# Performance work log

Hardware: AMD Instinct MI355X
Metric: run time of the kernel (lower is better)

Reference implementation:

```python
import jax, jax.numpy as jnp
import numpy as np

VOXEL_SIZE = np.array([0.2, 0.2, 4.0], dtype=np.float32)
PC_MIN = np.array([0.0, -40.0, -3.0], dtype=np.float32)
BN_EPS = 1e-3
N_POINTS = 1_500_000
N_VOXELS = 200_000
C_IN = 7   # (4 - 3) + 6 stats channels (cluster offset + voxel-center offset)
C_OUT = 64


def setup_inputs() -> dict:
    key = jax.random.key(0)
    ks = jax.random.split(key, 8)
    features = jax.random.normal(ks[0], (N_POINTS, 4), dtype=jnp.float32)
    point2voxel = jax.random.randint(ks[1], (N_POINTS,), 0, N_VOXELS).astype(jnp.int32)
    voxel_coors = jnp.stack([
        jax.random.randint(ks[2], (N_VOXELS,), 0, 2),    # batch idx
        jnp.zeros((N_VOXELS,), jnp.int32),               # z (pillars -> 0)
        jax.random.randint(ks[3], (N_VOXELS,), 0, 400),  # y bin
        jax.random.randint(ks[4], (N_VOXELS,), 0, 352),  # x bin
    ], axis=1).astype(jnp.int32)
    W = jax.random.normal(ks[5], (C_IN, C_OUT), dtype=jnp.float32) * 0.1
    bn_gamma = jnp.ones((C_OUT,), jnp.float32)
    bn_beta = jnp.zeros((C_OUT,), jnp.float32)
    bn_mean = jax.random.normal(ks[6], (C_OUT,), dtype=jnp.float32) * 0.01
    bn_var = jax.random.uniform(ks[7], (C_OUT,), minval=0.5, maxval=1.5, dtype=jnp.float32)
    return dict(features=features, W=W, bn_gamma=bn_gamma, bn_beta=bn_beta,
                bn_mean=bn_mean, bn_var=bn_var, point2voxel=point2voxel,
                voxel_coors=voxel_coors)


def reference(features, W, bn_gamma, bn_beta, bn_mean, bn_var, point2voxel, voxel_coors):
    M = voxel_coors.shape[0]
    xyz = features[:, :3]

    # --- stats: cluster-center offset (per-voxel mean of xyz, mapped back) ---
    cnt = jax.ops.segment_sum(jnp.ones((xyz.shape[0],), xyz.dtype), point2voxel,
                              num_segments=M)
    vmean = jax.ops.segment_sum(xyz, point2voxel, num_segments=M)
    vmean = vmean / jnp.maximum(cnt, 1.0)[:, None]
    cluster_off = xyz - vmean[point2voxel]

    # --- stats: voxel-center offset ---
    vs = jnp.asarray(VOXEL_SIZE)
    mn = jnp.asarray(PC_MIN)
    # coors layout is (batch, z, y, x) -> take (x, y, z)
    centers = (voxel_coors[:, jnp.array([3, 2, 1])].astype(jnp.float32) + 0.5) * vs + mn
    center_off = xyz - centers[point2voxel]

    feats = jnp.concatenate([cluster_off, center_off, features[:, 3:]], axis=-1)  # [N,7]

    # --- PFN layer: Linear(bias=False) + BN1d (eval stats) + ReLU ---
    h = feats @ W
    h = (h - bn_mean) * jax.lax.rsqrt(bn_var + BN_EPS) * bn_gamma + bn_beta
    h = jax.nn.relu(h)

    # --- scatter max-reduce to voxels ---
    vfeats = jax.ops.segment_max(h, point2voxel, num_segments=M)
    vfeats = jnp.where(jnp.isfinite(vfeats), vfeats, 0.0)  # guard rare empty voxels
    return vfeats, voxel_coors
```

## Files before the change

kernel.cpp:

```cpp
#include <hip/hip_runtime.h>


#define BBITS 7
#define BVOX  (1 << BBITS)
#define PCAP  1280
#define NR    (PCAP / 256)
#define NBLK  256
#define BMAX  1600
#define SCH   4096

__global__ __launch_bounds__(256) void hist_k(const int* __restrict__ p2v,
                                              int* __restrict__ mat,
                                              int N, int NB, int chunk) {
    __shared__ int h[BMAX];
    int b = blockIdx.x, tid = threadIdx.x;
    for (int k = tid; k < NB; k += 256) h[k] = 0;
    __syncthreads();
    int s = b * chunk, e = min(N, s + chunk);
    for (int i = s + tid; i < e; i += 256)
        atomicAdd(&h[p2v[i] >> BBITS], 1);
    __syncthreads();
    for (int k = tid; k < NB; k += 256) mat[b * NB + k] = h[k];
}

__global__ void scanA_k(int* __restrict__ mat, int* __restrict__ bsum,
                        int NB, int S) {
    __shared__ int s[256];
    int tid = threadIdx.x;
    int base = blockIdx.x * SCH + tid * 16;
    int idx[16], c[16];
    int tsum = 0;
#pragma unroll
    for (int j = 0; j < 16; ++j) {
        int p = base + j;
        if (p < S) {
            int k = p >> 8, b = p & 255;
            idx[j] = b * NB + k;
            c[j] = mat[idx[j]];
        } else {
            idx[j] = -1;
            c[j] = 0;
        }
        tsum += c[j];
    }
    s[tid] = tsum;
    __syncthreads();
    for (int off = 1; off < 256; off <<= 1) {
        int v = (tid >= off) ? s[tid - off] : 0;
        __syncthreads();
        s[tid] += v;
        __syncthreads();
    }
    int run = s[tid] - tsum;
#pragma unroll
    for (int j = 0; j < 16; ++j) {
        if (idx[j] >= 0) mat[idx[j]] = run;
        run += c[j];
    }
    if (tid == 255) bsum[blockIdx.x] = s[255];
}

__global__ void scanB_k(int* __restrict__ bsum, int nb) {
    __shared__ int s[256];
    int tid = threadIdx.x;
    int v = (tid < nb) ? bsum[tid] : 0;
    s[tid] = v;
    __syncthreads();
    for (int off = 1; off < 256; off <<= 1) {
        int t = (tid >= off) ? s[tid - off] : 0;
        __syncthreads();
        s[tid] += t;
        __syncthreads();
    }
    if (tid < nb) bsum[tid] = s[tid] - v;
}

__global__ __launch_bounds__(256) void scatter_kidx_k(const int* __restrict__ p2v,
                                                      const int* __restrict__ mat,
                                                      const int* __restrict__ bsum,
                                                      int* __restrict__ keyidx,
                                                      int N, int NB, int chunk) {
    __shared__ int cur[BMAX];
    int b = blockIdx.x, tid = threadIdx.x;
    for (int k = tid; k < NB; k += 256)
        cur[k] = mat[b * NB + k] + bsum[((k << 8) | b) >> 12];
    __syncthreads();
    int s = b * chunk, e = min(N, s + chunk);
    for (int i = s + tid; i < e; i += 256) {
        int v = p2v[i];
        int k = v >> BBITS;
        int pos = atomicAdd(&cur[k], 1);
        keyidx[pos] = (i << BBITS) | (v & (BVOX - 1));
    }
}

__global__ __launch_bounds__(256, 4) void gather_bucket_k(
    const float4* __restrict__ feats, const int* __restrict__ keyidx,
    const int* __restrict__ mat, const int* __restrict__ bsum,
    const float* __restrict__ W,
    const float* __restrict__ gamma, const float* __restrict__ beta,
    const float* __restrict__ mean, const float* __restrict__ var,
    const int* __restrict__ coors,
    float* __restrict__ out_v, float* __restrict__ out_c,
    int M, int NB, int N) {
    __shared__ float4 s_pay[PCAP];
    __shared__ int    s_cnt[BVOX];
    __shared__ int    s_off[BVOX];
    __shared__ int    s_cur[BVOX];
    __shared__ float4 s_cen[BVOX];

    int bk = blockIdx.x, tid = threadIdx.x;
    int lane = tid & 63, w = tid >> 6;

    float w0 = W[0 * 64 + lane], w1 = W[1 * 64 + lane], w2 = W[2 * 64 + lane];
    float w3 = W[3 * 64 + lane], w4 = W[4 * 64 + lane], w5 = W[5 * 64 + lane];
    float w6 = W[6 * 64 + lane];
    float sc = gamma[lane] * rsqrtf(var[lane] + 1e-3f);
    float bi = beta[lane] - mean[lane] * sc;
    float sgn = (sc >= 0.0f) ? 1.0f : -1.0f;
    float u0 = sgn * (w0 + w3), u1 = sgn * (w1 + w4);
    float u2 = sgn * (w2 + w5), u3 = sgn * w6;

    int s = mat[bk] + bsum[(bk << 8) >> 12];
    int e = (bk + 1 < NB) ? (mat[bk + 1] + bsum[((bk + 1) << 8) >> 12]) : N;
    int L = min(e - s, PCAP);

    int pk[NR];
    float4 fv[NR];
#pragma unroll
    for (int r = 0; r < NR; ++r) {
        int j = tid + r * 256;
        pk[r] = (j < L) ? keyidx[s + j] : -1;
    }
#pragma unroll
    for (int r = 0; r < NR; ++r)
        if (pk[r] >= 0) fv[r] = feats[pk[r] >> BBITS];

    if (tid < BVOX) s_cnt[tid] = 0;
    __syncthreads();
#pragma unroll
    for (int r = 0; r < NR; ++r)
        if (pk[r] >= 0) atomicAdd(&s_cnt[pk[r] & (BVOX - 1)], 1);

    int vbase = bk << BBITS;
    if (tid < BVOX) {
        int vg = vbase + tid;
        if (vg < M) {
            int4 cc = ((const int4*)coors)[vg];
            ((float4*)out_c)[vg] = make_float4((float)cc.x, (float)cc.y,
                                               (float)cc.z, (float)cc.w);
            s_cen[tid] = make_float4((cc.w + 0.5f) * 0.2f,
                                     (cc.z + 0.5f) * 0.2f - 40.0f,
                                     (cc.y + 0.5f) * 4.0f - 3.0f, 0.0f);
        }
    }
    __syncthreads();

    if (tid < BVOX) s_off[tid] = s_cnt[tid];
    __syncthreads();
    for (int off = 1; off < BVOX; off <<= 1) {
        int t = (tid < BVOX && tid >= off) ? s_off[tid - off] : 0;
        __syncthreads();
        if (tid < BVOX) s_off[tid] += t;
        __syncthreads();
    }
    if (tid < BVOX) {
        int ex = s_off[tid] - s_cnt[tid];
        s_off[tid] = ex;
        s_cur[tid] = ex;
    }
    __syncthreads();

#pragma unroll
    for (int r = 0; r < NR; ++r)
        if (pk[r] >= 0) {
            int vox = pk[r] & (BVOX - 1);
            int pos = atomicAdd(&s_cur[vox], 1);
            s_pay[pos] = fv[r];
        }
    __syncthreads();

    int lv0 = w << 5;
    int st = s_off[lv0];

    for (int q = 0; q < 32; ++q) {
        int lv = lv0 + q;
        int v = vbase + lv;
        int npts = s_cnt[lv];
        float4 cen = s_cen[lv];
        float sx = 0.f, sy = 0.f, sz = 0.f;
        float amax = -3.402823466e+38f;
        int i = 0;
        for (; i + 3 < npts; i += 4) {
            float4 f0 = s_pay[st + i + 0];
            float4 f1 = s_pay[st + i + 1];
            float4 f2 = s_pay[st + i + 2];
            float4 f3 = s_pay[st + i + 3];
            sx += f0.x + f1.x + f2.x + f3.x;
            sy += f0.y + f1.y + f2.y + f3.y;
            sz += f0.z + f1.z + f2.z + f3.z;
            float a0 = f0.x * u0 + f0.y * u1 + f0.z * u2 + f0.w * u3;
            float a1 = f1.x * u0 + f1.y * u1 + f1.z * u2 + f1.w * u3;
            float a2 = f2.x * u0 + f2.y * u1 + f2.z * u2 + f2.w * u3;
            float a3 = f3.x * u0 + f3.y * u1 + f3.z * u2 + f3.w * u3;
            amax = fmaxf(fmaxf(fmaxf(amax, a0), fmaxf(a1, a2)), a3);
        }
        for (; i < npts; ++i) {
            float4 f = s_pay[st + i];
            sx += f.x; sy += f.y; sz += f.z;
            float a = f.x * u0 + f.y * u1 + f.z * u2 + f.w * u3;
            amax = fmaxf(amax, a);
        }
        float res = 0.0f;
        if (npts > 0) {
            float inv = 1.0f / (float)npts;
            float mx = sx * inv, my = sy * inv, mz = sz * inv;
            float K = mx * w0 + my * w1 + mz * w2 +
                      cen.x * w3 + cen.y * w4 + cen.z * w5;
            float aext = sgn * amax;
            res = fmaxf((aext - K) * sc + bi, 0.0f);
        }
        if (v < M) out_v[(size_t)v * 64 + lane] = res;
        st += npts;
    }
}

extern "C" void kernel_launch(void* const* d_in, const int* in_sizes, int n_in,
                              void* d_out, int out_size, void* d_ws, size_t ws_size,
                              hipStream_t stream) {
    const float* features = (const float*)d_in[0];
    const float* W        = (const float*)d_in[1];
    const float* gamma    = (const float*)d_in[2];
    const float* beta     = (const float*)d_in[3];
    const float* mean     = (const float*)d_in[4];
    const float* var      = (const float*)d_in[5];
    const int*   p2v      = (const int*)d_in[6];
    const int*   coors    = (const int*)d_in[7];
    int N = in_sizes[0] / 4;
    int M = in_sizes[7] / 4;

    int NB = (M + BVOX - 1) >> BBITS;
    int S = NB * NBLK;
    int chunk = (N + NBLK - 1) / NBLK;

    int* mat    = (int*)d_ws;
    int* bsum   = mat + S;
    int* keyidx = bsum + 256;

    float* out_v = (float*)d_out;
    float* out_c = out_v + (size_t)M * 64;

    hist_k<<<NBLK, 256, 0, stream>>>(p2v, mat, N, NB, chunk);
    int nbA = (S + SCH - 1) / SCH;
    scanA_k<<<nbA, 256, 0, stream>>>(mat, bsum, NB, S);
    scanB_k<<<1, 256, 0, stream>>>(bsum, nbA);
    scatter_kidx_k<<<NBLK, 256, 0, stream>>>(p2v, mat, bsum, keyidx, N, NB, chunk);
    gather_bucket_k<<<NB, 256, 0, stream>>>(
        (const float4*)features, keyidx, mat, bsum, W, gamma, beta, mean, var,
        coors, out_v, out_c, M, NB, N);
}
```

Before: 125.6 us.

## Scatter feature payloads directly in bucket order and use wave-shuffle scan

The scatter pass now writes each point's float4 features and an 8-bit voxel id into bucket-sorted order, replacing the packed key/index array. The gather kernel then reads contiguous payloads instead of doing random feature loads through the index. The intra-block prefix scan now runs as a single-wave shuffle scan instead of a barrier-heavy shared-memory loop, and per-voxel counts are cached in registers. The histogram/scatter block count drops from 256 to 128. In exchange the scatter kernel does random 16-byte writes and the workspace grows by about 17 bytes per point.

```diff
diff --git a/kernel.cpp b/kernel.cpp
--- a/kernel.cpp
+++ b/kernel.cpp
@@ -1,13 +1,14 @@
 #include <hip/hip_runtime.h>
 
 
-#define BBITS 7
-#define BVOX  (1 << BBITS)
-#define PCAP  1280
-#define NR    (PCAP / 256)
-#define NBLK  256
-#define BMAX  1600
-#define SCH   4096
+#define BBITS  7
+#define BVOX   (1 << BBITS)
+#define PCAP   1280
+#define NR     (PCAP / 256)
+#define NBBITS 7
+#define NBLK   (1 << NBBITS)
+#define BMAX   1600
+#define SCH    4096
 
 __global__ __launch_bounds__(256) void hist_k(const int* __restrict__ p2v,
                                               int* __restrict__ mat,
@@ -34,7 +35,7 @@
     for (int j = 0; j < 16; ++j) {
         int p = base + j;
         if (p < S) {
-            int k = p >> 8, b = p & 255;
+            int k = p >> NBBITS, b = p & (NBLK - 1);
             idx[j] = b * NB + k;
             c[j] = mat[idx[j]];
         } else {
@@ -75,27 +76,28 @@
     if (tid < nb) bsum[tid] = s[tid] - v;
 }
 
-__global__ __launch_bounds__(256) void scatter_kidx_k(const int* __restrict__ p2v,
-                                                      const int* __restrict__ mat,
-                                                      const int* __restrict__ bsum,
-                                                      int* __restrict__ keyidx,
-                                                      int N, int NB, int chunk) {
+__global__ __launch_bounds__(256) void scatter_pay_k(
+    const int* __restrict__ p2v, const float4* __restrict__ feats,
+    const int* __restrict__ mat, const int* __restrict__ bsum,
+    float4* __restrict__ pay, unsigned char* __restrict__ voxid,
+    int N, int NB, int chunk) {
     __shared__ int cur[BMAX];
     int b = blockIdx.x, tid = threadIdx.x;
     for (int k = tid; k < NB; k += 256)
-        cur[k] = mat[b * NB + k] + bsum[((k << 8) | b) >> 12];
+        cur[k] = mat[b * NB + k] + bsum[((k << NBBITS) | b) >> 12];
     __syncthreads();
     int s = b * chunk, e = min(N, s + chunk);
     for (int i = s + tid; i < e; i += 256) {
         int v = p2v[i];
         int k = v >> BBITS;
         int pos = atomicAdd(&cur[k], 1);
-        keyidx[pos] = (i << BBITS) | (v & (BVOX - 1));
+        pay[pos] = feats[i];
+        voxid[pos] = (unsigned char)(v & (BVOX - 1));
     }
 }
 
 __global__ __launch_bounds__(256, 4) void gather_bucket_k(
-    const float4* __restrict__ feats, const int* __restrict__ keyidx,
+    const float4* __restrict__ pay, const unsigned char* __restrict__ voxid,
     const int* __restrict__ mat, const int* __restrict__ bsum,
     const float* __restrict__ W,
     const float* __restrict__ gamma, const float* __restrict__ beta,
@@ -121,26 +123,28 @@
     float u0 = sgn * (w0 + w3), u1 = sgn * (w1 + w4);
     float u2 = sgn * (w2 + w5), u3 = sgn * w6;
 
-    int s = mat[bk] + bsum[(bk << 8) >> 12];
-    int e = (bk + 1 < NB) ? (mat[bk + 1] + bsum[((bk + 1) << 8) >> 12]) : N;
+    int s = mat[bk] + bsum[(bk << NBBITS) >> 12];
+    int e = (bk + 1 < NB) ? (mat[bk + 1] + bsum[((bk + 1) << NBBITS) >> 12]) : N;
     int L = min(e - s, PCAP);
 
-    int pk[NR];
     float4 fv[NR];
+    int vx[NR];
 #pragma unroll
     for (int r = 0; r < NR; ++r) {
         int j = tid + r * 256;
-        pk[r] = (j < L) ? keyidx[s + j] : -1;
-    }
+        if (j < L) {
+            fv[r] = pay[s + j];
+            vx[r] = voxid[s + j];
+        } else {
+            vx[r] = -1;
+        }
+    }
+
+    if (tid < BVOX) s_cnt[tid] = 0;
+    __syncthreads();
 #pragma unroll
     for (int r = 0; r < NR; ++r)
-        if (pk[r] >= 0) fv[r] = feats[pk[r] >> BBITS];
-
-    if (tid < BVOX) s_cnt[tid] = 0;
-    __syncthreads();
-#pragma unroll
-    for (int r = 0; r < NR; ++r)
-        if (pk[r] >= 0) atomicAdd(&s_cnt[pk[r] & (BVOX - 1)], 1);
+        if (vx[r] >= 0) atomicAdd(&s_cnt[vx[r]], 1);
 
     int vbase = bk << BBITS;
     if (tid < BVOX) {
@@ -156,37 +160,41 @@
     }
     __syncthreads();
 
-    if (tid < BVOX) s_off[tid] = s_cnt[tid];
-    __syncthreads();
-    for (int off = 1; off < BVOX; off <<= 1) {
-        int t = (tid < BVOX && tid >= off) ? s_off[tid - off] : 0;
-        __syncthreads();
-        if (tid < BVOX) s_off[tid] += t;
-        __syncthreads();
-    }
-    if (tid < BVOX) {
-        int ex = s_off[tid] - s_cnt[tid];
-        s_off[tid] = ex;
-        s_cur[tid] = ex;
+    if (w == 0) {
+        int c0 = s_cnt[2 * lane], c1 = s_cnt[2 * lane + 1];
+        int cp = c0 + c1;
+        int x = cp;
+        for (int off = 1; off < 64; off <<= 1) {
+            int t = __shfl_up(x, off);
+            if (lane >= off) x += t;
+        }
+        int ex = x - cp;
+        s_off[2 * lane] = ex;
+        s_off[2 * lane + 1] = ex + c0;
+        s_cur[2 * lane] = ex;
+        s_cur[2 * lane + 1] = ex + c0;
     }
     __syncthreads();
 
 #pragma unroll
     for (int r = 0; r < NR; ++r)
-        if (pk[r] >= 0) {
-            int vox = pk[r] & (BVOX - 1);
-            int pos = atomicAdd(&s_cur[vox], 1);
+        if (vx[r] >= 0) {
+            int pos = atomicAdd(&s_cur[vx[r]], 1);
             s_pay[pos] = fv[r];
         }
     __syncthreads();
 
     int lv0 = w << 5;
+    int cnts[32];
+#pragma unroll
+    for (int q = 0; q < 32; ++q) cnts[q] = s_cnt[lv0 + q];
     int st = s_off[lv0];
 
+#pragma unroll
     for (int q = 0; q < 32; ++q) {
         int lv = lv0 + q;
         int v = vbase + lv;
-        int npts = s_cnt[lv];
+        int npts = cnts[q];
         float4 cen = s_cen[lv];
         float sx = 0.f, sy = 0.f, sz = 0.f;
         float amax = -3.402823466e+38f;
@@ -243,9 +251,10 @@
     int S = NB * NBLK;
     int chunk = (N + NBLK - 1) / NBLK;
 
-    int* mat    = (int*)d_ws;
-    int* bsum   = mat + S;
-    int* keyidx = bsum + 256;
+    float4* pay           = (float4*)d_ws;
+    unsigned char* voxid  = (unsigned char*)(pay + N);
+    int* mat              = (int*)(voxid + ((N + 3) & ~3));
+    int* bsum             = mat + S;
 
     float* out_v = (float*)d_out;
     float* out_c = out_v + (size_t)M * 64;
@@ -254,8 +263,9 @@
     int nbA = (S + SCH - 1) / SCH;
     scanA_k<<<nbA, 256, 0, stream>>>(mat, bsum, NB, S);
     scanB_k<<<1, 256, 0, stream>>>(bsum, nbA);
-    scatter_kidx_k<<<NBLK, 256, 0, stream>>>(p2v, mat, bsum, keyidx, N, NB, chunk);
+    scatter_pay_k<<<NBLK, 256, 0, stream>>>(
+        p2v, (const float4*)features, mat, bsum, pay, voxid, N, NB, chunk);
     gather_bucket_k<<<NB, 256, 0, stream>>>(
-        (const float4*)features, keyidx, mat, bsum, W, gamma, beta, mean, var,
+        pay, voxid, mat, bsum, W, gamma, beta, mean, var,
         coors, out_v, out_c, M, NB, N);
 }
```

Result: slower. 135.5 us (median of 2 runs) (+7.9%).
